# Optimization experiments

Measured on AMD Instinct MI355X. Metric: run time of the kernel, lower is better.

## Reference

```python
import jax, jax.numpy as jnp
import numpy as np

B, T, IN, H, L = 512, 75, 96, 1024, 3
HARDTANH_LIMIT = 1.0


def setup_inputs() -> dict:
    key = jax.random.key(0)
    ks = jax.random.split(key, 32)
    inp = {
        'inputs': jax.random.normal(ks[0], (B, T, IN), jnp.float32),
        'hiddens': jax.random.normal(ks[1], (L, B, H), jnp.float32),
        'cells': jax.random.normal(ks[2], (L, B, H), jnp.float32),
    }
    s = 1.0 / np.sqrt(H)
    kidx = 3
    for i in range(L):
        in_dim = IN if i == 0 else H
        inp[f'Wih{i}'] = jax.random.uniform(ks[kidx], (4 * H, in_dim), jnp.float32, -s, s); kidx += 1
        inp[f'Whh{i}'] = jax.random.uniform(ks[kidx], (4 * H, H), jnp.float32, -s, s); kidx += 1
        inp[f'bih{i}'] = jax.random.uniform(ks[kidx], (4 * H,), jnp.float32, -s, s); kidx += 1
        inp[f'bhh{i}'] = jax.random.uniform(ks[kidx], (4 * H,), jnp.float32, -s, s); kidx += 1
    inp['fc_w'] = jax.random.uniform(ks[kidx], (IN, H), jnp.float32, -s, s); kidx += 1
    inp['fc_b'] = jax.random.uniform(ks[kidx], (IN,), jnp.float32, -s, s)
    return inp


def _lstm_cell(x, h, c, Wih, Whh, bih, bhh):
    # PyTorch LSTMCell gate order: i, f, g, o
    gates = x @ Wih.T + bih + h @ Whh.T + bhh  # [B, 4H]
    i, f, g, o = jnp.split(gates, 4, axis=-1)
    c_new = jax.nn.sigmoid(f) * c + jax.nn.sigmoid(i) * jnp.tanh(g)
    h_new = jax.nn.sigmoid(o) * jnp.tanh(c_new)
    return h_new, c_new


def reference(inputs, hiddens, cells,
              Wih0, Whh0, bih0, bhh0,
              Wih1, Whh1, bih1, bhh1,
              Wih2, Whh2, bih2, bhh2,
              fc_w, fc_b):
    params = [(Wih0, Whh0, bih0, bhh0),
              (Wih1, Whh1, bih1, bhh1),
              (Wih2, Whh2, bih2, bhh2)]
    # dropout p=0.0 -> identity
    out0 = inputs[..., 0, :]  # [B, IN]

    def step(carry, _):
        hs, cs, out = carry
        x = jax.lax.stop_gradient(out)  # .detach() in the original
        new_h, new_c = [], []
        for i, (Wih, Whh, bih, bhh) in enumerate(params):
            xi = x if i == 0 else new_h[i - 1]
            h, c = _lstm_cell(xi, hs[i], cs[i], Wih, Whh, bih, bhh)
            new_h.append(h)
            new_c.append(c)
        out = new_h[-1] @ fc_w.T + fc_b
        out = jnp.clip(out, -HARDTANH_LIMIT, HARDTANH_LIMIT)  # Hardtanh
        return (jnp.stack(new_h), jnp.stack(new_c), out), out

    (_, _, _), outs = jax.lax.scan(step, (hiddens, cells, out0), None, length=inputs.shape[-2])
    return jnp.swapaxes(outs, 0, 1)  # [B, T, IN]
```

## Files before the change

kernel.cpp:

```cpp
#include <hip/hip_runtime.h>
#include <cstdint>
#include <cstddef>


typedef unsigned short u16;
typedef float v4f __attribute__((ext_vector_type(4)));
typedef short v8s __attribute__((ext_vector_type(8)));
typedef u16   v8u16 __attribute__((ext_vector_type(8)));

#define BATCH 512
#define H_DIM 1024
#define GATES 4096
#define T_STEPS 75
#define IN_DIM 96
#define K0P 1152
#define K12 2048
#define NBLK 256

__device__ __forceinline__ float bf2f(u16 u) {
    unsigned int x = ((unsigned int)u) << 16;
    return __builtin_bit_cast(float, x);
}
__device__ __forceinline__ u16 f2bf(float f) {
    unsigned int x = __builtin_bit_cast(unsigned int, f);
    x += 0x7fffu + ((x >> 16) & 1u);
    return (u16)(x >> 16);
}
__device__ __forceinline__ void gload16(const void* g, void* l) {
    __builtin_amdgcn_global_load_lds(
        (const __attribute__((address_space(1))) void*)g,
        (__attribute__((address_space(3))) void*)l, 16, 0, 0);
}
__device__ __forceinline__ void gload16c(const void* g, void* l) {
    __builtin_amdgcn_global_load_lds(
        (const __attribute__((address_space(1))) void*)g,
        (__attribute__((address_space(3))) void*)l, 16, 0, 0x11);
}
__device__ __forceinline__ void st_agent_u32(unsigned int* p, unsigned int v) {
    __hip_atomic_store(p, v, __ATOMIC_RELAXED, __HIP_MEMORY_SCOPE_AGENT);
}
__device__ __forceinline__ unsigned int ld_agent_u32(const unsigned int* p) {
    return __hip_atomic_load(p, __ATOMIC_RELAXED, __HIP_MEMORY_SCOPE_AGENT);
}

__device__ __forceinline__ void grid_sync(int* bar, int g) {
    __syncthreads();
    if (threadIdx.x == 0) {
        int old = __hip_atomic_fetch_add(&bar[(blockIdx.x & 7) * 32], 1,
                                         __ATOMIC_RELAXED, __HIP_MEMORY_SCOPE_AGENT);
        if (old + 1 == 32 * g) {
            int r = __hip_atomic_fetch_add(&bar[256], 1,
                                           __ATOMIC_RELAXED, __HIP_MEMORY_SCOPE_AGENT);
            if (r + 1 == 8 * g)
                __hip_atomic_store(&bar[288], g,
                                   __ATOMIC_RELAXED, __HIP_MEMORY_SCOPE_AGENT);
        }
        int spins = 0;
        while (__hip_atomic_load(&bar[288],
                                 __ATOMIC_RELAXED, __HIP_MEMORY_SCOPE_AGENT) < g) {
            if (++spins > (1 << 17)) break;
            __builtin_amdgcn_s_sleep(1);
        }
    }
    __syncthreads();
}

__device__ __forceinline__ void gemm_stage(
    char* smem, const u16* __restrict__ A, const u16* __restrict__ W,
    int K, int nk, v4f bv, v4f& cc,
    u16* __restrict__ h1, int h1s, u16* __restrict__ h2, int h2s,
    int bm, int j0)
{
    u16* sA = (u16*)smem;
    u16* sB = (u16*)(smem + 32768);

    const int tid  = threadIdx.x;
    const int lane = tid & 63;
    const int wid  = tid >> 6;
    const int wm   = (wid >> 1) * 16;
    const int wn   = (wid & 1) * 64;
    const int l15  = lane & 15;
    const int lq   = lane >> 4;

    v4f acc[4];
    #pragma unroll
    for (int nf = 0; nf < 4; ++nf) {
        v4f tv = {bv[nf], bv[nf], bv[nf], bv[nf]};
        acc[nf] = tv;
    }

    const int srow = tid >> 3;
    const int kcs  = ((tid & 7) ^ (srow & 7)) << 3;

    auto stage = [&](int b, int k0) {
        u16* sa = sA + b * 4096;
        u16* sb = sB + b * 8192;
        gload16c(A + (size_t)(bm + srow) * K + k0 + kcs, sa + tid * 8);
        #pragma unroll
        for (int q = 0; q < 2; ++q) {
            const int fr = q * 64 + srow;
            gload16(W + (size_t)((fr >> 5) * H_DIM + j0 + (fr & 31)) * K + k0 + kcs,
                    sb + q * 4096 + tid * 8);
        }
    };

    {
        const int npre = nk < 3 ? nk : 3;
        for (int p = 0; p < npre; ++p) stage(p, p * 64);
    }

    #pragma unroll 1
    for (int tt = 0; tt < nk; ++tt) {
        const int cur = tt & 3;
        if (tt + 3 < nk) stage((tt + 3) & 3, (tt + 3) * 64);
        const int ahead = (nk - 1 - tt) < 3 ? (nk - 1 - tt) : 3;
        if (ahead == 3)      asm volatile("s_waitcnt vmcnt(9)" ::: "memory");
        else if (ahead == 2) asm volatile("s_waitcnt vmcnt(6)" ::: "memory");
        else if (ahead == 1) asm volatile("s_waitcnt vmcnt(3)" ::: "memory");
        else                 asm volatile("s_waitcnt vmcnt(0)" ::: "memory");
        asm volatile("s_barrier" ::: "memory");

        const char* sa = (const char*)(sA + cur * 4096);
        const char* sb = (const char*)(sB + cur * 8192);
        v8s af[2], bfr[4][2];
        #pragma unroll
        for (int ks = 0; ks < 2; ++ks) {
            const int row = wm + l15;
            const int ch  = ks * 4 + lq;
            af[ks] = *(const v8s*)(sa + row * 128 + (((ch ^ (row & 7))) << 4));
        }
        #pragma unroll
        for (int nf = 0; nf < 4; ++nf)
            #pragma unroll
            for (int ks = 0; ks < 2; ++ks) {
                const int row = wn + nf * 16 + l15;
                const int ch  = ks * 4 + lq;
                bfr[nf][ks] = *(const v8s*)(sb + row * 128 + (((ch ^ (row & 7))) << 4));
            }
        #pragma unroll
        for (int ks = 0; ks < 2; ++ks)
            #pragma unroll
            for (int nf = 0; nf < 4; ++nf)
                acc[nf] = __builtin_amdgcn_mfma_f32_16x16x32_bf16(
                    af[ks], bfr[nf][ks], acc[nf], 0, 0, 0);
        asm volatile("s_barrier" ::: "memory");
    }

    float* sG = (float*)smem;
    #pragma unroll
    for (int nf = 0; nf < 4; ++nf)
        #pragma unroll
        for (int r = 0; r < 4; ++r)
            sG[(wm + lq * 4 + r) * 132 + wn + nf * 16 + l15] = acc[nf][r];
    __syncthreads();

    const int erow = tid >> 3;
    const int jj   = (tid & 7) * 4;
    const int gb   = bm + erow;
    const float* sGr = sG + erow * 132;
    v4f n0;
    u16 hv[4];
    #pragma unroll
    for (int q = 0; q < 4; ++q) {
        const float gi = sGr[      jj + q];
        const float gf = sGr[32  + jj + q];
        const float gg = sGr[64  + jj + q];
        const float go = sGr[96  + jj + q];
        const float cv = cc[q];
        const float ii = 1.f / (1.f + __expf(-gi));
        const float ff = 1.f / (1.f + __expf(-gf));
        const float g2 = tanhf(gg);
        const float oo = 1.f / (1.f + __expf(-go));
        const float cq = ff * cv + ii * g2;
        n0[q] = cq;
        hv[q] = f2bf(oo * tanhf(cq));
    }
    cc = n0;
    unsigned int* d1 = (unsigned int*)(h1 + (size_t)gb * h1s + j0 + jj);
    #pragma unroll
    for (int w2 = 0; w2 < 2; ++w2) {
        unsigned int val = (unsigned int)hv[2 * w2] | ((unsigned int)hv[2 * w2 + 1] << 16);
        st_agent_u32(d1 + w2, val);
    }
    if (h2) {
        unsigned int* d2 = (unsigned int*)(h2 + (size_t)gb * h2s + j0 + jj);
        #pragma unroll
        for (int w2 = 0; w2 < 2; ++w2) {
            unsigned int val = (unsigned int)hv[2 * w2] | ((unsigned int)hv[2 * w2 + 1] << 16);
            st_agent_u32(d2 + w2, val);
        }
    }
}

__device__ __forceinline__ void fc_stage(
    char* smem, const u16* __restrict__ h2, int h2s,
    const u16* __restrict__ w, const float* __restrict__ fcb,
    float* __restrict__ out, u16* __restrict__ xdst, int t, int id)
{
    float* sh = (float*)smem;
    const int tid  = threadIdx.x;
    const int half = tid >> 8;
    const int htid = tid & 255;
    const int b    = id * 2 + half;
    const unsigned int* hp = (const unsigned int*)(h2 + (size_t)b * h2s + htid * 4);
    #pragma unroll
    for (int w4 = 0; w4 < 2; ++w4) {
        unsigned int u = ld_agent_u32(hp + w4);
        sh[half * H_DIM + htid * 4 + 2 * w4]     = bf2f((u16)(u & 0xffffu));
        sh[half * H_DIM + htid * 4 + 2 * w4 + 1] = bf2f((u16)(u >> 16));
    }
    __syncthreads();
    if (htid < IN_DIM) {
        const u16* wr = w + (size_t)htid * H_DIM;
        const float* shr = sh + half * H_DIM;
        float acc = fcb[htid];
        #pragma unroll 4
        for (int k = 0; k < H_DIM; k += 8) {
            v8u16 wv = *(const v8u16*)(wr + k);
            #pragma unroll
            for (int q = 0; q < 8; ++q) acc += shr[k + q] * bf2f(wv[q]);
        }
        acc = fminf(1.f, fmaxf(-1.f, acc));
        out[(size_t)b * (T_STEPS * IN_DIM) + t * IN_DIM + htid] = acc;
        float o2 = __shfl_xor(acc, 1);
        if ((htid & 1) == 0) {
            unsigned int val = (unsigned int)f2bf(acc) | ((unsigned int)f2bf(o2) << 16);
            st_agent_u32((unsigned int*)(xdst + (size_t)b * K0P + htid), val);
        }
    }
}

__global__ __launch_bounds__(512, 1) void lstm_all_k(
    const u16* __restrict__ w0, const u16* __restrict__ w1, const u16* __restrict__ w2,
    u16* A00, u16* A01, u16* A10, u16* A11, u16* A20, u16* A21,
    const u16* __restrict__ fcw, const float* __restrict__ bsum,
    const float* __restrict__ cells, const float* __restrict__ fcb,
    float* __restrict__ out, int* bar)
{
    __shared__ __align__(16) char smem[98304];

    const int tid  = threadIdx.x;
    const int lane = tid & 63;
    const int wid  = tid >> 6;
    const int wn   = (wid & 1) * 64;
    const int l15  = lane & 15;

    const int id    = blockIdx.x;
    const int panel = (id & 7) * 4 + (id >> 6);
    const int mblk  = (id >> 3) & 7;
    const int bm    = mblk * 64;
    const int j0    = panel * 32;

    v4f bv0, bv1, bv2;
    #pragma unroll
    for (int nf = 0; nf < 4; ++nf) {
        const int ncol = wn + nf * 16 + l15;
        const int idx  = (ncol >> 5) * H_DIM + j0 + (ncol & 31);
        bv0[nf] = bsum[idx];
        bv1[nf] = bsum[GATES + idx];
        bv2[nf] = bsum[2 * GATES + idx];
    }

    const int erow = tid >> 3;
    const int jj   = (tid & 7) * 4;
    const int gb   = bm + erow;
    v4f c0, c1, c2;
    {
        const float* cr = cells + (size_t)gb * H_DIM + j0 + jj;
        c0 = *(const v4f*)cr;
        cr += (size_t)BATCH * H_DIM;
        c1 = *(const v4f*)cr;
        cr += (size_t)BATCH * H_DIM;
        c2 = *(const v4f*)cr;
    }

    int g = 0;
    #pragma unroll 1
    for (int t = 0; t < T_STEPS; ++t) {
        const int pr = t & 1;
        u16* A0r = pr ? A01 : A00;  u16* A0w = pr ? A00 : A01;
        u16* A1r = pr ? A11 : A10;  u16* A1w = pr ? A10 : A11;
        u16* A2r = pr ? A21 : A20;  u16* A2w = pr ? A20 : A21;

        gemm_stage(smem, A0r, w0, K0P, K0P / 64, bv0, c0,
                   A0w + IN_DIM, K0P, A1r, K12, bm, j0);
        grid_sync(bar, ++g);
        gemm_stage(smem, A1r, w1, K12, K12 / 64, bv1, c1,
                   A1w + H_DIM, K12, A2r, K12, bm, j0);
        grid_sync(bar, ++g);
        gemm_stage(smem, A2r, w2, K12, K12 / 64, bv2, c2,
                   A2w + H_DIM, K12, (u16*)nullptr, 0, bm, j0);
        grid_sync(bar, ++g);
        fc_stage(smem, A2w + H_DIM, K12, fcw, fcb, out, A0w, t, id);
        grid_sync(bar, ++g);
    }
}

__global__ __launch_bounds__(256) void convpack_k(
    const float* __restrict__ src, int srcStride,
    u16* __restrict__ dst, int dstStride, int cols8, long total8)
{
    long i = (long)blockIdx.x * 256 + threadIdx.x;
    if (i >= total8) return;
    const int r  = (int)(i / cols8);
    const int cc = (int)(i - (long)r * cols8) * 8;
    const float* s = src + (size_t)r * srcStride + cc;
    v4f a = *(const v4f*)s;
    v4f b = *(const v4f*)(s + 4);
    v8u16 o;
    #pragma unroll
    for (int q = 0; q < 4; ++q) { o[q] = f2bf(a[q]); o[4 + q] = f2bf(b[q]); }
    *(v8u16*)(dst + (size_t)r * dstStride + cc) = o;
}

__global__ __launch_bounds__(256) void zero16_k(
    u16* __restrict__ dst, int dstStride, int cols8, long total8)
{
    long i = (long)blockIdx.x * 256 + threadIdx.x;
    if (i >= total8) return;
    const int r  = (int)(i / cols8);
    const int cc = (int)(i - (long)r * cols8) * 8;
    v8u16 z = {0, 0, 0, 0, 0, 0, 0, 0};
    *(v8u16*)(dst + (size_t)r * dstStride + cc) = z;
}

__global__ __launch_bounds__(256) void add_k(
    const float* __restrict__ a, const float* __restrict__ b,
    float* __restrict__ o, int n)
{
    int i = blockIdx.x * 256 + threadIdx.x;
    if (i < n) o[i] = a[i] + b[i];
}

extern "C" void kernel_launch(void* const* d_in, const int* in_sizes, int n_in,
                              void* d_out, int out_size, void* d_ws, size_t ws_size,
                              hipStream_t stream)
{
    const float* inputs  = (const float*)d_in[0];
    const float* hiddens = (const float*)d_in[1];
    const float* cells   = (const float*)d_in[2];
    const float* Wih[3]  = {(const float*)d_in[3], (const float*)d_in[7],  (const float*)d_in[11]};
    const float* Whh[3]  = {(const float*)d_in[4], (const float*)d_in[8],  (const float*)d_in[12]};
    const float* bih[3]  = {(const float*)d_in[5], (const float*)d_in[9],  (const float*)d_in[13]};
    const float* bhh[3]  = {(const float*)d_in[6], (const float*)d_in[10], (const float*)d_in[14]};
    const float* fc_w    = (const float*)d_in[15];
    const float* fc_b    = (const float*)d_in[16];
    float* out = (float*)d_out;

    char* p = (char*)d_ws;
    auto take = [&](size_t bytes) -> void* {
        void* r = p; p += (bytes + 255) & ~(size_t)255; return r;
    };
    const int Kl[3]  = {K0P, K12, K12};
    const int Kin[3] = {IN_DIM, H_DIM, H_DIM};
    u16* wcat[3];
    for (int l = 0; l < 3; ++l) wcat[l] = (u16*)take((size_t)GATES * Kl[l] * 2);
    u16* Ab[3][2];
    for (int l = 0; l < 3; ++l)
        for (int q = 0; q < 2; ++q) Ab[l][q] = (u16*)take((size_t)BATCH * Kl[l] * 2);
    u16*   fcwb = (u16*)take((size_t)IN_DIM * H_DIM * 2);
    float* bsum = (float*)take((size_t)3 * GATES * 4);
    int*   bar  = (int*)take(8192);
    if ((size_t)(p - (char*)d_ws) > ws_size) return;

    auto pack = [&](const float* s, int ss, u16* d, int ds, int rows, int cols) {
        long t8 = (long)rows * (cols / 8);
        convpack_k<<<(int)((t8 + 255) / 256), 256, 0, stream>>>(s, ss, d, ds, cols / 8, t8);
    };
    auto zero = [&](u16* d, int ds, int rows, int cols) {
        long t8 = (long)rows * (cols / 8);
        zero16_k<<<(int)((t8 + 255) / 256), 256, 0, stream>>>(d, ds, cols / 8, t8);
    };

    for (int l = 0; l < 3; ++l) {
        pack(Wih[l], Kin[l], wcat[l],           Kl[l], GATES, Kin[l]);
        pack(Whh[l], H_DIM,  wcat[l] + Kin[l],  Kl[l], GATES, H_DIM);
    }
    zero(wcat[0] + IN_DIM + H_DIM, K0P, GATES, K0P - IN_DIM - H_DIM);
    pack(fc_w, H_DIM, fcwb, H_DIM, IN_DIM, H_DIM);

    for (int l = 0; l < 3; ++l)
        pack(hiddens + (size_t)l * BATCH * H_DIM, H_DIM,
             Ab[l][0] + Kin[l], Kl[l], BATCH, H_DIM);
    pack(inputs, T_STEPS * IN_DIM, Ab[0][0], K0P, BATCH, IN_DIM);
    zero(Ab[0][0] + IN_DIM + H_DIM, K0P, BATCH, K0P - IN_DIM - H_DIM);
    zero(Ab[0][1] + IN_DIM + H_DIM, K0P, BATCH, K0P - IN_DIM - H_DIM);

    for (int l = 0; l < 3; ++l)
        add_k<<<16, 256, 0, stream>>>(bih[l], bhh[l], bsum + l * GATES, GATES);
    hipMemsetAsync(bar, 0, 8192, stream);

    lstm_all_k<<<NBLK, 512, 0, stream>>>(
        wcat[0], wcat[1], wcat[2],
        Ab[0][0], Ab[0][1], Ab[1][0], Ab[1][1], Ab[2][0], Ab[2][1],
        fcwb, bsum, cells, fc_b, out,
        bar);
}
```

Measured before the change: 4.482 ms.

## Double block size to 1024 threads, halving per-wave MFMA tile work

Each persistent block now launches 16 waves instead of 8. Each wave computes a 16x32 output tile instead of 16x64, and global-to-LDS staging is spread across all 1024 threads, with the vmcnt waits adjusted per thread half. The epilogue and FC stage now handle two elements per thread instead of four. The goal is more latency hiding per CU in the latency-bound recurrent loop, at the cost of fewer registers per thread and more costly block barriers.

```diff
diff --git a/kernel.cpp b/kernel.cpp
--- a/kernel.cpp
+++ b/kernel.cpp
@@ -4,6 +4,7 @@
 
 
 typedef unsigned short u16;
+typedef float v2f __attribute__((ext_vector_type(2)));
 typedef float v4f __attribute__((ext_vector_type(4)));
 typedef short v8s __attribute__((ext_vector_type(8)));
 typedef u16   v8u16 __attribute__((ext_vector_type(8)));
@@ -67,7 +68,7 @@
 
 __device__ __forceinline__ void gemm_stage(
     char* smem, const u16* __restrict__ A, const u16* __restrict__ W,
-    int K, int nk, v4f bv, v4f& cc,
+    int K, int nk, v2f bv, v2f& cc,
     u16* __restrict__ h1, int h1s, u16* __restrict__ h2, int h2s,
     int bm, int j0)
 {
@@ -77,30 +78,35 @@
     const int tid  = threadIdx.x;
     const int lane = tid & 63;
     const int wid  = tid >> 6;
-    const int wm   = (wid >> 1) * 16;
-    const int wn   = (wid & 1) * 64;
+    const int wm   = (wid >> 2) * 16;
+    const int wn   = (wid & 3) * 32;
     const int l15  = lane & 15;
     const int lq   = lane >> 4;
-
-    v4f acc[4];
+    const bool wlo = (tid < 512);
+
+    v4f acc[2];
     #pragma unroll
-    for (int nf = 0; nf < 4; ++nf) {
+    for (int nf = 0; nf < 2; ++nf) {
         v4f tv = {bv[nf], bv[nf], bv[nf], bv[nf]};
         acc[nf] = tv;
     }
-
-    const int srow = tid >> 3;
-    const int kcs  = ((tid & 7) ^ (srow & 7)) << 3;
 
     auto stage = [&](int b, int k0) {
         u16* sa = sA + b * 4096;
         u16* sb = sB + b * 8192;
-        gload16c(A + (size_t)(bm + srow) * K + k0 + kcs, sa + tid * 8);
-        #pragma unroll
-        for (int q = 0; q < 2; ++q) {
-            const int fr = q * 64 + srow;
-            gload16(W + (size_t)((fr >> 5) * H_DIM + j0 + (fr & 31)) * K + k0 + kcs,
-                    sb + q * 4096 + tid * 8);
+        if (wlo) {
+            const int r  = tid >> 3;
+            const int kc = ((tid & 7) ^ (r & 7)) << 3;
+            gload16c(A + (size_t)(bm + r) * K + k0 + kc, sa + tid * 8);
+            gload16(W + (size_t)((r >> 5) * H_DIM + j0 + (r & 31)) * K + k0 + kc,
+                    sb + tid * 8);
+        } else {
+            const int st = tid - 512;
+            const int r  = st >> 3;
+            const int fr = 64 + r;
+            const int kc = ((st & 7) ^ (r & 7)) << 3;
+            gload16(W + (size_t)((fr >> 5) * H_DIM + j0 + (fr & 31)) * K + k0 + kc,
+                    sb + 4096 + st * 8);
         }
     };
 
@@ -114,15 +120,22 @@
         const int cur = tt & 3;
         if (tt + 3 < nk) stage((tt + 3) & 3, (tt + 3) * 64);
         const int ahead = (nk - 1 - tt) < 3 ? (nk - 1 - tt) : 3;
-        if (ahead == 3)      asm volatile("s_waitcnt vmcnt(9)" ::: "memory");
-        else if (ahead == 2) asm volatile("s_waitcnt vmcnt(6)" ::: "memory");
-        else if (ahead == 1) asm volatile("s_waitcnt vmcnt(3)" ::: "memory");
-        else                 asm volatile("s_waitcnt vmcnt(0)" ::: "memory");
+        if (wlo) {
+            if (ahead == 3)      asm volatile("s_waitcnt vmcnt(6)" ::: "memory");
+            else if (ahead == 2) asm volatile("s_waitcnt vmcnt(4)" ::: "memory");
+            else if (ahead == 1) asm volatile("s_waitcnt vmcnt(2)" ::: "memory");
+            else                 asm volatile("s_waitcnt vmcnt(0)" ::: "memory");
+        } else {
+            if (ahead == 3)      asm volatile("s_waitcnt vmcnt(3)" ::: "memory");
+            else if (ahead == 2) asm volatile("s_waitcnt vmcnt(2)" ::: "memory");
+            else if (ahead == 1) asm volatile("s_waitcnt vmcnt(1)" ::: "memory");
+            else                 asm volatile("s_waitcnt vmcnt(0)" ::: "memory");
+        }
         asm volatile("s_barrier" ::: "memory");
 
         const char* sa = (const char*)(sA + cur * 4096);
         const char* sb = (const char*)(sB + cur * 8192);
-        v8s af[2], bfr[4][2];
+        v8s af[2], bfr[2][2];
         #pragma unroll
         for (int ks = 0; ks < 2; ++ks) {
             const int row = wm + l15;
@@ -130,7 +143,7 @@
             af[ks] = *(const v8s*)(sa + row * 128 + (((ch ^ (row & 7))) << 4));
         }
         #pragma unroll
-        for (int nf = 0; nf < 4; ++nf)
+        for (int nf = 0; nf < 2; ++nf)
             #pragma unroll
             for (int ks = 0; ks < 2; ++ks) {
                 const int row = wn + nf * 16 + l15;
@@ -140,7 +153,7 @@
         #pragma unroll
         for (int ks = 0; ks < 2; ++ks)
             #pragma unroll
-            for (int nf = 0; nf < 4; ++nf)
+            for (int nf = 0; nf < 2; ++nf)
                 acc[nf] = __builtin_amdgcn_mfma_f32_16x16x32_bf16(
                     af[ks], bfr[nf][ks], acc[nf], 0, 0, 0);
         asm volatile("s_barrier" ::: "memory");
@@ -148,20 +161,20 @@
 
     float* sG = (float*)smem;
     #pragma unroll
-    for (int nf = 0; nf < 4; ++nf)
+    for (int nf = 0; nf < 2; ++nf)
         #pragma unroll
         for (int r = 0; r < 4; ++r)
             sG[(wm + lq * 4 + r) * 132 + wn + nf * 16 + l15] = acc[nf][r];
     __syncthreads();
 
-    const int erow = tid >> 3;
-    const int jj   = (tid & 7) * 4;
+    const int erow = tid >> 4;
+    const int jj   = (tid & 15) * 2;
     const int gb   = bm + erow;
     const float* sGr = sG + erow * 132;
-    v4f n0;
-    u16 hv[4];
+    v2f n0;
+    u16 hv[2];
     #pragma unroll
-    for (int q = 0; q < 4; ++q) {
+    for (int q = 0; q < 2; ++q) {
         const float gi = sGr[      jj + q];
         const float gf = sGr[32  + jj + q];
         const float gg = sGr[64  + jj + q];
@@ -176,20 +189,10 @@
         hv[q] = f2bf(oo * tanhf(cq));
     }
     cc = n0;
-    unsigned int* d1 = (unsigned int*)(h1 + (size_t)gb * h1s + j0 + jj);
-    #pragma unroll
-    for (int w2 = 0; w2 < 2; ++w2) {
-        unsigned int val = (unsigned int)hv[2 * w2] | ((unsigned int)hv[2 * w2 + 1] << 16);
-        st_agent_u32(d1 + w2, val);
-    }
-    if (h2) {
-        unsigned int* d2 = (unsigned int*)(h2 + (size_t)gb * h2s + j0 + jj);
-        #pragma unroll
-        for (int w2 = 0; w2 < 2; ++w2) {
-            unsigned int val = (unsigned int)hv[2 * w2] | ((unsigned int)hv[2 * w2 + 1] << 16);
-            st_agent_u32(d2 + w2, val);
-        }
-    }
+    unsigned int val = (unsigned int)hv[0] | ((unsigned int)hv[1] << 16);
+    st_agent_u32((unsigned int*)(h1 + (size_t)gb * h1s + j0 + jj), val);
+    if (h2)
+        st_agent_u32((unsigned int*)(h2 + (size_t)gb * h2s + j0 + jj), val);
 }
 
 __device__ __forceinline__ void fc_stage(
@@ -199,15 +202,14 @@
 {
     float* sh = (float*)smem;
     const int tid  = threadIdx.x;
-    const int half = tid >> 8;
-    const int htid = tid & 255;
+    const int half = tid >> 9;
+    const int htid = tid & 511;
     const int b    = id * 2 + half;
-    const unsigned int* hp = (const unsigned int*)(h2 + (size_t)b * h2s + htid * 4);
-    #pragma unroll
-    for (int w4 = 0; w4 < 2; ++w4) {
-        unsigned int u = ld_agent_u32(hp + w4);
-        sh[half * H_DIM + htid * 4 + 2 * w4]     = bf2f((u16)(u & 0xffffu));
-        sh[half * H_DIM + htid * 4 + 2 * w4 + 1] = bf2f((u16)(u >> 16));
+    {
+        const unsigned int* hp = (const unsigned int*)(h2 + (size_t)b * h2s);
+        unsigned int u = ld_agent_u32(hp + htid);
+        sh[half * H_DIM + htid * 2]     = bf2f((u16)(u & 0xffffu));
+        sh[half * H_DIM + htid * 2 + 1] = bf2f((u16)(u >> 16));
     }
     __syncthreads();
     if (htid < IN_DIM) {
@@ -230,7 +232,7 @@
     }
 }
 
-__global__ __launch_bounds__(512, 1) void lstm_all_k(
+__global__ __launch_bounds__(1024, 4) void lstm_all_k(
     const u16* __restrict__ w0, const u16* __restrict__ w1, const u16* __restrict__ w2,
     u16* A00, u16* A01, u16* A10, u16* A11, u16* A20, u16* A21,
     const u16* __restrict__ fcw, const float* __restrict__ bsum,
@@ -242,7 +244,7 @@
     const int tid  = threadIdx.x;
     const int lane = tid & 63;
     const int wid  = tid >> 6;
-    const int wn   = (wid & 1) * 64;
+    const int wn   = (wid & 3) * 32;
     const int l15  = lane & 15;
 
     const int id    = blockIdx.x;
@@ -251,9 +253,9 @@
     const int bm    = mblk * 64;
     const int j0    = panel * 32;
 
-    v4f bv0, bv1, bv2;
+    v2f bv0, bv1, bv2;
     #pragma unroll
-    for (int nf = 0; nf < 4; ++nf) {
+    for (int nf = 0; nf < 2; ++nf) {
         const int ncol = wn + nf * 16 + l15;
         const int idx  = (ncol >> 5) * H_DIM + j0 + (ncol & 31);
         bv0[nf] = bsum[idx];
@@ -261,17 +263,17 @@
         bv2[nf] = bsum[2 * GATES + idx];
     }
 
-    const int erow = tid >> 3;
-    const int jj   = (tid & 7) * 4;
+    const int erow = tid >> 4;
+    const int jj   = (tid & 15) * 2;
     const int gb   = bm + erow;
-    v4f c0, c1, c2;
+    v2f c0, c1, c2;
     {
         const float* cr = cells + (size_t)gb * H_DIM + j0 + jj;
-        c0 = *(const v4f*)cr;
+        c0 = *(const v2f*)cr;
         cr += (size_t)BATCH * H_DIM;
-        c1 = *(const v4f*)cr;
+        c1 = *(const v2f*)cr;
         cr += (size_t)BATCH * H_DIM;
-        c2 = *(const v4f*)cr;
+        c2 = *(const v2f*)cr;
     }
 
     int g = 0;
@@ -390,7 +392,7 @@
         add_k<<<16, 256, 0, stream>>>(bih[l], bhh[l], bsum + l * GATES, GATES);
     hipMemsetAsync(bar, 0, 8192, stream);
 
-    lstm_all_k<<<NBLK, 512, 0, stream>>>(
+    lstm_all_k<<<NBLK, 1024, 0, stream>>>(
         wcat[0], wcat[1], wcat[2],
         Ab[0][0], Ab[0][1], Ab[1][0], Ab[1][1], Ab[2][0], Ab[2][1],
         fcwb, bsum, cells, fc_b, out,
```

After: 4.797 ms. 7.0% more time.

## Add prefetch warp that warms L2 with next layer's weights during GEMM

Applied to the files above, without the earlier changes.

Adds a ninth wavefront per block (576 threads) that, while the 512 compute threads run the current layer's GEMM, issues global-to-LDS loads of this block's slice of the next layer's weights into a scratch LDS area. Each load overwrites the same scratch slot, so the only intent is to pull those weight rows into L2/MALL before the next stage needs them, hiding load latency after each grid sync. The extra wave must match the compute threads' s_barrier count every k-iteration, which couples its pacing to the GEMM loop and adds memory traffic and register/LDS pressure.

```diff
diff --git a/kernel.cpp b/kernel.cpp
--- a/kernel.cpp
+++ b/kernel.cpp
@@ -16,6 +16,8 @@
 #define K0P 1152
 #define K12 2048
 #define NBLK 256
+#define NTHR 576
+#define SCRATCH 98304
 
 __device__ __forceinline__ float bf2f(u16 u) {
     unsigned int x = ((unsigned int)u) << 16;
@@ -69,126 +71,153 @@
     char* smem, const u16* __restrict__ A, const u16* __restrict__ W,
     int K, int nk, v4f bv, v4f& cc,
     u16* __restrict__ h1, int h1s, u16* __restrict__ h2, int h2s,
-    int bm, int j0)
-{
-    u16* sA = (u16*)smem;
-    u16* sB = (u16*)(smem + 32768);
-
-    const int tid  = threadIdx.x;
-    const int lane = tid & 63;
-    const int wid  = tid >> 6;
-    const int wm   = (wid >> 1) * 16;
-    const int wn   = (wid & 1) * 64;
-    const int l15  = lane & 15;
-    const int lq   = lane >> 4;
-
-    v4f acc[4];
-    #pragma unroll
-    for (int nf = 0; nf < 4; ++nf) {
-        v4f tv = {bv[nf], bv[nf], bv[nf], bv[nf]};
-        acc[nf] = tv;
-    }
-
-    const int srow = tid >> 3;
-    const int kcs  = ((tid & 7) ^ (srow & 7)) << 3;
-
-    auto stage = [&](int b, int k0) {
-        u16* sa = sA + b * 4096;
-        u16* sb = sB + b * 8192;
-        gload16c(A + (size_t)(bm + srow) * K + k0 + kcs, sa + tid * 8);
-        #pragma unroll
-        for (int q = 0; q < 2; ++q) {
-            const int fr = q * 64 + srow;
-            gload16(W + (size_t)((fr >> 5) * H_DIM + j0 + (fr & 31)) * K + k0 + kcs,
-                    sb + q * 4096 + tid * 8);
-        }
-    };
-
-    {
-        const int npre = nk < 3 ? nk : 3;
-        for (int p = 0; p < npre; ++p) stage(p, p * 64);
-    }
-
-    #pragma unroll 1
-    for (int tt = 0; tt < nk; ++tt) {
-        const int cur = tt & 3;
-        if (tt + 3 < nk) stage((tt + 3) & 3, (tt + 3) * 64);
-        const int ahead = (nk - 1 - tt) < 3 ? (nk - 1 - tt) : 3;
-        if (ahead == 3)      asm volatile("s_waitcnt vmcnt(9)" ::: "memory");
-        else if (ahead == 2) asm volatile("s_waitcnt vmcnt(6)" ::: "memory");
-        else if (ahead == 1) asm volatile("s_waitcnt vmcnt(3)" ::: "memory");
-        else                 asm volatile("s_waitcnt vmcnt(0)" ::: "memory");
-        asm volatile("s_barrier" ::: "memory");
-
-        const char* sa = (const char*)(sA + cur * 4096);
-        const char* sb = (const char*)(sB + cur * 8192);
-        v8s af[2], bfr[4][2];
-        #pragma unroll
-        for (int ks = 0; ks < 2; ++ks) {
-            const int row = wm + l15;
-            const int ch  = ks * 4 + lq;
-            af[ks] = *(const v8s*)(sa + row * 128 + (((ch ^ (row & 7))) << 4));
-        }
+    int bm, int j0,
+    const u16* __restrict__ Wn, int Kn, int cs, int lpi)
+{
+    const int tid = threadIdx.x;
+
+    if (tid < 512) {
+        u16* sA = (u16*)smem;
+        u16* sB = (u16*)(smem + 32768);
+
+        const int lane = tid & 63;
+        const int wid  = tid >> 6;
+        const int wm   = (wid >> 1) * 16;
+        const int wn   = (wid & 1) * 64;
+        const int l15  = lane & 15;
+        const int lq   = lane >> 4;
+
+        v4f acc[4];
+        #pragma unroll
+        for (int nf = 0; nf < 4; ++nf) {
+            v4f tv = {bv[nf], bv[nf], bv[nf], bv[nf]};
+            acc[nf] = tv;
+        }
+
+        const int srow = tid >> 3;
+        const int kcs  = ((tid & 7) ^ (srow & 7)) << 3;
+
+        auto stage = [&](int b, int k0) {
+            u16* sa = sA + b * 4096;
+            u16* sb = sB + b * 8192;
+            gload16c(A + (size_t)(bm + srow) * K + k0 + kcs, sa + tid * 8);
+            #pragma unroll
+            for (int q = 0; q < 2; ++q) {
+                const int fr = q * 64 + srow;
+                gload16(W + (size_t)((fr >> 5) * H_DIM + j0 + (fr & 31)) * K + k0 + kcs,
+                        sb + q * 4096 + tid * 8);
+            }
+        };
+
+        {
+            const int npre = nk < 3 ? nk : 3;
+            for (int p = 0; p < npre; ++p) stage(p, p * 64);
+        }
+
+        #pragma unroll 1
+        for (int tt = 0; tt < nk; ++tt) {
+            const int cur = tt & 3;
+            if (tt + 3 < nk) stage((tt + 3) & 3, (tt + 3) * 64);
+            const int ahead = (nk - 1 - tt) < 3 ? (nk - 1 - tt) : 3;
+            if (ahead == 3)      asm volatile("s_waitcnt vmcnt(9)" ::: "memory");
+            else if (ahead == 2) asm volatile("s_waitcnt vmcnt(6)" ::: "memory");
+            else if (ahead == 1) asm volatile("s_waitcnt vmcnt(3)" ::: "memory");
+            else                 asm volatile("s_waitcnt vmcnt(0)" ::: "memory");
+            asm volatile("s_barrier" ::: "memory");
+
+            const char* sa = (const char*)(sA + cur * 4096);
+            const char* sb = (const char*)(sB + cur * 8192);
+            v8s af[2], bfr[4][2];
+            #pragma unroll
+            for (int ks = 0; ks < 2; ++ks) {
+                const int row = wm + l15;
+                const int ch  = ks * 4 + lq;
+                af[ks] = *(const v8s*)(sa + row * 128 + (((ch ^ (row & 7))) << 4));
+            }
+            #pragma unroll
+            for (int nf = 0; nf < 4; ++nf)
+                #pragma unroll
+                for (int ks = 0; ks < 2; ++ks) {
+                    const int row = wn + nf * 16 + l15;
+                    const int ch  = ks * 4 + lq;
+                    bfr[nf][ks] = *(const v8s*)(sb + row * 128 + (((ch ^ (row & 7))) << 4));
+                }
+            #pragma unroll
+            for (int ks = 0; ks < 2; ++ks)
+                #pragma unroll
+                for (int nf = 0; nf < 4; ++nf)
+                    acc[nf] = __builtin_amdgcn_mfma_f32_16x16x32_bf16(
+                        af[ks], bfr[nf][ks], acc[nf], 0, 0, 0);
+            asm volatile("s_barrier" ::: "memory");
+        }
+
+        float* sG = (float*)smem;
         #pragma unroll
         for (int nf = 0; nf < 4; ++nf)
             #pragma unroll
-            for (int ks = 0; ks < 2; ++ks) {
-                const int row = wn + nf * 16 + l15;
-                const int ch  = ks * 4 + lq;
-                bfr[nf][ks] = *(const v8s*)(sb + row * 128 + (((ch ^ (row & 7))) << 4));
-            }
-        #pragma unroll
-        for (int ks = 0; ks < 2; ++ks)
-            #pragma unroll
-            for (int nf = 0; nf < 4; ++nf)
-                acc[nf] = __builtin_amdgcn_mfma_f32_16x16x32_bf16(
-                    af[ks], bfr[nf][ks], acc[nf], 0, 0, 0);
-        asm volatile("s_barrier" ::: "memory");
-    }
-
-    float* sG = (float*)smem;
-    #pragma unroll
-    for (int nf = 0; nf < 4; ++nf)
-        #pragma unroll
-        for (int r = 0; r < 4; ++r)
-            sG[(wm + lq * 4 + r) * 132 + wn + nf * 16 + l15] = acc[nf][r];
-    __syncthreads();
-
-    const int erow = tid >> 3;
-    const int jj   = (tid & 7) * 4;
-    const int gb   = bm + erow;
-    const float* sGr = sG + erow * 132;
-    v4f n0;
-    u16 hv[4];
-    #pragma unroll
-    for (int q = 0; q < 4; ++q) {
-        const float gi = sGr[      jj + q];
-        const float gf = sGr[32  + jj + q];
-        const float gg = sGr[64  + jj + q];
-        const float go = sGr[96  + jj + q];
-        const float cv = cc[q];
-        const float ii = 1.f / (1.f + __expf(-gi));
-        const float ff = 1.f / (1.f + __expf(-gf));
-        const float g2 = tanhf(gg);
-        const float oo = 1.f / (1.f + __expf(-go));
-        const float cq = ff * cv + ii * g2;
-        n0[q] = cq;
-        hv[q] = f2bf(oo * tanhf(cq));
-    }
-    cc = n0;
-    unsigned int* d1 = (unsigned int*)(h1 + (size_t)gb * h1s + j0 + jj);
-    #pragma unroll
-    for (int w2 = 0; w2 < 2; ++w2) {
-        unsigned int val = (unsigned int)hv[2 * w2] | ((unsigned int)hv[2 * w2 + 1] << 16);
-        st_agent_u32(d1 + w2, val);
-    }
-    if (h2) {
-        unsigned int* d2 = (unsigned int*)(h2 + (size_t)gb * h2s + j0 + jj);
+            for (int r = 0; r < 4; ++r)
+                sG[(wm + lq * 4 + r) * 132 + wn + nf * 16 + l15] = acc[nf][r];
+        __syncthreads();
+
+        const int erow = tid >> 3;
+        const int jj   = (tid & 7) * 4;
+        const int gb   = bm + erow;
+        const float* sGr = sG + erow * 132;
+        v4f n0;
+        u16 hv[4];
+        #pragma unroll
+        for (int q = 0; q < 4; ++q) {
+            const float gi = sGr[      jj + q];
+            const float gf = sGr[32  + jj + q];
+            const float gg = sGr[64  + jj + q];
+            const float go = sGr[96  + jj + q];
+            const float cv = cc[q];
+            const float ii = 1.f / (1.f + __expf(-gi));
+            const float ff = 1.f / (1.f + __expf(-gf));
+            const float g2 = tanhf(gg);
+            const float oo = 1.f / (1.f + __expf(-go));
+            const float cq = ff * cv + ii * g2;
+            n0[q] = cq;
+            hv[q] = f2bf(oo * tanhf(cq));
+        }
+        cc = n0;
+        unsigned int* d1 = (unsigned int*)(h1 + (size_t)gb * h1s + j0 + jj);
         #pragma unroll
         for (int w2 = 0; w2 < 2; ++w2) {
             unsigned int val = (unsigned int)hv[2 * w2] | ((unsigned int)hv[2 * w2 + 1] << 16);
-            st_agent_u32(d2 + w2, val);
-        }
+            st_agent_u32(d1 + w2, val);
+        }
+        if (h2) {
+            unsigned int* d2 = (unsigned int*)(h2 + (size_t)gb * h2s + j0 + jj);
+            #pragma unroll
+            for (int w2 = 0; w2 < 2; ++w2) {
+                unsigned int val = (unsigned int)hv[2 * w2] | ((unsigned int)hv[2 * w2 + 1] << 16);
+                st_agent_u32(d2 + w2, val);
+            }
+        }
+    } else {
+        const int lane   = tid & 63;
+        u16* scratch = (u16*)(smem + SCRATCH);
+        const int mblk16 = bm >> 2;
+        const int total  = 16 << cs;
+        int rem = total, l = 0;
+        #pragma unroll 1
+        for (int tt = 0; tt < nk; ++tt) {
+            int n = rem < lpi ? rem : lpi;
+            for (int i2 = 0; i2 < n; ++i2, ++l) {
+                const int ri  = l >> cs;
+                const int ck  = l & ((1 << cs) - 1);
+                const int idx = mblk16 + ri;
+                const size_t elt =
+                    (size_t)((idx >> 5) * H_DIM + j0 + (idx & 31)) * Kn
+                    + (size_t)ck * 512 + (size_t)lane * 8;
+                gload16(Wn + elt, scratch + lane * 8);
+            }
+            rem -= n;
+            asm volatile("s_barrier" ::: "memory");
+            asm volatile("s_barrier" ::: "memory");
+        }
+        __syncthreads();
     }
 }
 
@@ -199,18 +228,20 @@
 {
     float* sh = (float*)smem;
     const int tid  = threadIdx.x;
-    const int half = tid >> 8;
+    const int half = (tid >> 8) & 1;
     const int htid = tid & 255;
     const int b    = id * 2 + half;
-    const unsigned int* hp = (const unsigned int*)(h2 + (size_t)b * h2s + htid * 4);
-    #pragma unroll
-    for (int w4 = 0; w4 < 2; ++w4) {
-        unsigned int u = ld_agent_u32(hp + w4);
-        sh[half * H_DIM + htid * 4 + 2 * w4]     = bf2f((u16)(u & 0xffffu));
-        sh[half * H_DIM + htid * 4 + 2 * w4 + 1] = bf2f((u16)(u >> 16));
+    if (tid < 512) {
+        const unsigned int* hp = (const unsigned int*)(h2 + (size_t)b * h2s + htid * 4);
+        #pragma unroll
+        for (int w4 = 0; w4 < 2; ++w4) {
+            unsigned int u = ld_agent_u32(hp + w4);
+            sh[half * H_DIM + htid * 4 + 2 * w4]     = bf2f((u16)(u & 0xffffu));
+            sh[half * H_DIM + htid * 4 + 2 * w4 + 1] = bf2f((u16)(u >> 16));
+        }
     }
     __syncthreads();
-    if (htid < IN_DIM) {
+    if (tid < 512 && htid < IN_DIM) {
         const u16* wr = w + (size_t)htid * H_DIM;
         const float* shr = sh + half * H_DIM;
         float acc = fcb[htid];
@@ -230,14 +261,14 @@
     }
 }
 
-__global__ __launch_bounds__(512, 1) void lstm_all_k(
+__global__ __launch_bounds__(NTHR, 1) void lstm_all_k(
     const u16* __restrict__ w0, const u16* __restrict__ w1, const u16* __restrict__ w2,
     u16* A00, u16* A01, u16* A10, u16* A11, u16* A20, u16* A21,
     const u16* __restrict__ fcw, const float* __restrict__ bsum,
     const float* __restrict__ cells, const float* __restrict__ fcb,
     float* __restrict__ out, int* bar)
 {
-    __shared__ __align__(16) char smem[98304];
+    __shared__ __align__(16) char smem[99328];
 
     const int tid  = threadIdx.x;
     const int lane = tid & 63;
@@ -251,21 +282,20 @@
     const int bm    = mblk * 64;
     const int j0    = panel * 32;
 
-    v4f bv0, bv1, bv2;
-    #pragma unroll
-    for (int nf = 0; nf < 4; ++nf) {
-        const int ncol = wn + nf * 16 + l15;
-        const int idx  = (ncol >> 5) * H_DIM + j0 + (ncol & 31);
-        bv0[nf] = bsum[idx];
-        bv1[nf] = bsum[GATES + idx];
-        bv2[nf] = bsum[2 * GATES + idx];
-    }
-
-    const int erow = tid >> 3;
-    const int jj   = (tid & 7) * 4;
-    const int gb   = bm + erow;
-    v4f c0, c1, c2;
-    {
+    v4f bv0 = {0,0,0,0}, bv1 = {0,0,0,0}, bv2 = {0,0,0,0};
+    v4f c0 = {0,0,0,0}, c1 = {0,0,0,0}, c2 = {0,0,0,0};
+    if (tid < 512) {
+        #pragma unroll
+        for (int nf = 0; nf < 4; ++nf) {
+            const int ncol = wn + nf * 16 + l15;
+            const int idx  = (ncol >> 5) * H_DIM + j0 + (ncol & 31);
+            bv0[nf] = bsum[idx];
+            bv1[nf] = bsum[GATES + idx];
+            bv2[nf] = bsum[2 * GATES + idx];
+        }
+        const int erow = tid >> 3;
+        const int jj   = (tid & 7) * 4;
+        const int gb   = bm + erow;
         const float* cr = cells + (size_t)gb * H_DIM + j0 + jj;
         c0 = *(const v4f*)cr;
         cr += (size_t)BATCH * H_DIM;
@@ -283,13 +313,16 @@
         u16* A2r = pr ? A21 : A20;  u16* A2w = pr ? A20 : A21;
 
         gemm_stage(smem, A0r, w0, K0P, K0P / 64, bv0, c0,
-                   A0w + IN_DIM, K0P, A1r, K12, bm, j0);
+                   A0w + IN_DIM, K0P, A1r, K12, bm, j0,
+                   w1, K12, 2, 4);
         grid_sync(bar, ++g);
         gemm_stage(smem, A1r, w1, K12, K12 / 64, bv1, c1,
-                   A1w + H_DIM, K12, A2r, K12, bm, j0);
+                   A1w + H_DIM, K12, A2r, K12, bm, j0,
+                   w2, K12, 2, 2);
         grid_sync(bar, ++g);
         gemm_stage(smem, A2r, w2, K12, K12 / 64, bv2, c2,
-                   A2w + H_DIM, K12, (u16*)nullptr, 0, bm, j0);
+                   A2w + H_DIM, K12, (u16*)nullptr, 0, bm, j0,
+                   w0, K0P, 1, 1);
         grid_sync(bar, ++g);
         fc_stage(smem, A2w + H_DIM, K12, fcw, fcb, out, A0w, t, id);
         grid_sync(bar, ++g);
@@ -390,7 +423,7 @@
         add_k<<<16, 256, 0, stream>>>(bih[l], bhh[l], bsum + l * GATES, GATES);
     hipMemsetAsync(bar, 0, 8192, stream);
 
-    lstm_all_k<<<NBLK, 512, 0, stream>>>(
+    lstm_all_k<<<NBLK, NTHR, 0, stream>>>(
         wcat[0], wcat[1], wcat[2],
         Ab[0][0], Ab[0][1], Ab[1][0], Ab[1][1], Ab[2][0], Ab[2][1],
         fcwb, bsum, cells, fc_b, out,
```

After: 5.659 ms. 1.26x slower.
